# Optimization experiments

Measured on AMD Instinct MI355X. Metric: run time of the kernel, lower is better.

Reference implementation:

```python
import jax, jax.numpy as jnp
import numpy as np

VOCAB = 50257
EMBED_DIM = 768


def setup_inputs() -> dict:
    key = jax.random.key(0)
    k1, k2 = jax.random.split(key)
    x = jax.random.randint(k1, (8, 2048), 0, VOCAB, dtype=jnp.int64 if jax.config.jax_enable_x64 else jnp.int32)
    weight = jax.random.normal(k2, (EMBED_DIM, VOCAB), dtype=jnp.float32)
    return {"x": x, "weight": weight}


def reference(x, weight):
    # Original: one_hot(x, vocab) @ weight.T  ==  gather rows of weight.T
    # weight: [embed_dim, vocab]; output: [batch, seq, embed_dim]
    return jnp.take(weight.T, x, axis=0)
```

## Files before the change

### kernel.cpp

```cpp
#include <hip/hip_runtime.h>


#define VOCAB 50257
#define EMBED 768
#define WINB 32
#define NWIN 1571
#define NWIN_P 2048
#define RG 4
#define ROWS 192
#define LSTRIDE 33
#define CHUNK 256

__global__ __launch_bounds__(1024) void hist_scan_kernel(const int* __restrict__ x,
                                                         int n,
                                                         int* __restrict__ off,
                                                         int* __restrict__ cur) {
  __shared__ int h[NWIN_P];
  __shared__ int b[NWIN_P];
  const int t = threadIdx.x;
  h[t] = 0; h[t + 1024] = 0;
  __syncthreads();
  for (int i = t; i < n; i += 1024) atomicAdd(&h[x[i] >> 5], 1);
  __syncthreads();
  int* src = h; int* dst = b;
  for (int d = 1; d < NWIN_P; d <<= 1) {
    for (int i = t; i < NWIN_P; i += 1024)
      dst[i] = (i >= d) ? src[i] + src[i - d] : src[i];
    __syncthreads();
    int* tmp = src; src = dst; dst = tmp;
  }
  for (int i = t; i < NWIN_P; i += 1024) {
    int e = (i > 0) ? src[i - 1] : 0;
    off[i] = e;
    cur[i] = e;
  }
}

__global__ __launch_bounds__(256) void scatter_kernel(const int* __restrict__ x,
                                                      int* __restrict__ cur,
                                                      int* __restrict__ sorted,
                                                      int n) {
  int i = blockIdx.x * blockDim.x + threadIdx.x;
  if (i < n) {
    int v = x[i];
    int p = atomicAdd(&cur[v >> 5], 1);
    sorted[p] = (i << 5) | (v & 31);
  }
}

__device__ __forceinline__ int xcd_swizzle(int bid, int nwg) {
  const int NX = 8;
  int q = nwg / NX, r = nwg % NX;
  int xcd = bid % NX, idx = bid / NX;
  int base = (xcd < r) ? xcd * (q + 1) : r * (q + 1) + (xcd - r) * q;
  return base + idx;
}

__global__ __launch_bounds__(256) void gather_kernel(const float* __restrict__ w,
                                                     const int* __restrict__ off,
                                                     const int* __restrict__ sorted,
                                                     float* __restrict__ out) {
  __shared__ float lds[ROWS * LSTRIDE];
  __shared__ int toks[CHUNK];
  const int logical = xcd_swizzle(blockIdx.x, NWIN * RG);
  const int wid = logical % NWIN;
  const int rg  = logical / NWIN;
  const int row0 = rg * ROWS;
  const int col0 = wid * WINB;
  const int tid = threadIdx.x;

  int beg = off[wid], end = off[wid + 1];

  if (wid != NWIN - 1) {
    #pragma unroll
    for (int j = tid; j < ROWS * 8; j += 256) {
      int r = j >> 3, c4 = (j & 7) << 2;
      float4 v = *(const float4*)&w[(size_t)(row0 + r) * VOCAB + col0 + c4];
      float* d = &lds[r * LSTRIDE + c4];
      d[0] = v.x; d[1] = v.y; d[2] = v.z; d[3] = v.w;
    }
  } else {
    for (int j = tid; j < ROWS * 8; j += 256) {
      int r = j >> 3, c4 = (j & 7) << 2;
      float* d = &lds[r * LSTRIDE + c4];
      for (int u = 0; u < 4; ++u) {
        int c = col0 + c4 + u;
        d[u] = (c < VOCAB) ? w[(size_t)(row0 + r) * VOCAB + c] : 0.f;
      }
    }
  }

  int m = end - beg; if (m > CHUNK) m = CHUNK;
  if (tid < m) toks[tid] = sorted[beg + tid];
  __syncthreads();

  const int wave = tid >> 6, lane = tid & 63;
  while (true) {
    for (int i = wave; i < m; i += 4) {
      int pk = toks[i];
      int t = pk >> 5, c = pk & 31;
      float* o = &out[(size_t)t * EMBED + row0];
      #pragma unroll
      for (int k = 0; k < 3; ++k)
        o[k * 64 + lane] = lds[(k * 64 + lane) * LSTRIDE + c];
    }
    beg += m;
    if (beg >= end) break;
    __syncthreads();
    m = end - beg; if (m > CHUNK) m = CHUNK;
    if (tid < m) toks[tid] = sorted[beg + tid];
    __syncthreads();
  }
}

extern "C" void kernel_launch(void* const* d_in, const int* in_sizes, int n_in,
                              void* d_out, int out_size, void* d_ws, size_t ws_size,
                              hipStream_t stream) {
  const int*   x = (const int*)d_in[0];
  const float* w = (const float*)d_in[1];
  float* out = (float*)d_out;
  const int n = in_sizes[0];

  int* off    = (int*)d_ws;
  int* cur    = off + NWIN_P + 1;
  int* sorted = cur + NWIN_P;

  hist_scan_kernel<<<1, 1024, 0, stream>>>(x, n, off, cur);
  scatter_kernel<<<(n + 255) / 256, 256, 0, stream>>>(x, cur, sorted, n);
  gather_kernel<<<NWIN * RG, 256, 0, stream>>>(w, off, sorted, out);
}
```

Measured before the change: 52.51 us.

## Load weight tiles with direct global-to-LDS loads and XOR-swizzled layout

The gather kernel now stages weight tiles into LDS with global_load_lds 16-byte direct loads instead of register round-trips. The padded stride is replaced by an XOR swizzle to avoid bank conflicts, and the tile shrinks to 128 rows across 6 row groups. The histogram moves from one single-block kernel to a grid-wide atomic kernel plus a separate scan kernel and a memset. This adds two launches and relies on the direct-to-LDS lane/address mapping being correct.

Result: slower. 56.27 us (+7.2%).

```diff
diff --git a/kernel.cpp b/kernel.cpp
--- a/kernel.cpp
+++ b/kernel.cpp
@@ -6,23 +6,25 @@
 #define WINB 32
 #define NWIN 1571
 #define NWIN_P 2048
-#define RG 4
-#define ROWS 192
-#define LSTRIDE 33
+#define RG 6
+#define ROWS 128
 #define CHUNK 256
 
-__global__ __launch_bounds__(1024) void hist_scan_kernel(const int* __restrict__ x,
-                                                         int n,
-                                                         int* __restrict__ off,
-                                                         int* __restrict__ cur) {
-  __shared__ int h[NWIN_P];
-  __shared__ int b[NWIN_P];
-  const int t = threadIdx.x;
-  h[t] = 0; h[t + 1024] = 0;
+__global__ __launch_bounds__(256) void hist_kernel(const int* __restrict__ x,
+                                                   int* __restrict__ cnt, int n) {
+  int i = blockIdx.x * blockDim.x + threadIdx.x;
+  if (i < n) atomicAdd(&cnt[x[i] >> 5], 1);
+}
+
+__global__ __launch_bounds__(1024) void scan_kernel(const int* __restrict__ cnt,
+                                                    int* __restrict__ off,
+                                                    int* __restrict__ cur) {
+  __shared__ int a[NWIN_P], b[NWIN_P];
+  int t = threadIdx.x;
+  a[t] = cnt[t];
+  a[t + 1024] = cnt[t + 1024];
   __syncthreads();
-  for (int i = t; i < n; i += 1024) atomicAdd(&h[x[i] >> 5], 1);
-  __syncthreads();
-  int* src = h; int* dst = b;
+  int* src = a; int* dst = b;
   for (int d = 1; d < NWIN_P; d <<= 1) {
     for (int i = t; i < NWIN_P; i += 1024)
       dst[i] = (i >= d) ? src[i] + src[i - d] : src[i];
@@ -60,7 +62,7 @@
                                                      const int* __restrict__ off,
                                                      const int* __restrict__ sorted,
                                                      float* __restrict__ out) {
-  __shared__ float lds[ROWS * LSTRIDE];
+  __shared__ float lds[ROWS * WINB];
   __shared__ int toks[CHUNK];
   const int logical = xcd_swizzle(blockIdx.x, NWIN * RG);
   const int wid = logical % NWIN;
@@ -68,25 +70,28 @@
   const int row0 = rg * ROWS;
   const int col0 = wid * WINB;
   const int tid = threadIdx.x;
+  const int wave = tid >> 6, lane = tid & 63;
 
   int beg = off[wid], end = off[wid + 1];
 
   if (wid != NWIN - 1) {
     #pragma unroll
-    for (int j = tid; j < ROWS * 8; j += 256) {
-      int r = j >> 3, c4 = (j & 7) << 2;
-      float4 v = *(const float4*)&w[(size_t)(row0 + r) * VOCAB + col0 + c4];
-      float* d = &lds[r * LSTRIDE + c4];
-      d[0] = v.x; d[1] = v.y; d[2] = v.z; d[3] = v.w;
+    for (int k = 0; k < ROWS * 8 / 256; ++k) {
+      int p = k * 256 + tid;
+      int r = p >> 3;
+      int c4 = (p & 7) ^ ((r >> 2) & 7);
+      const float* src = &w[(size_t)(row0 + r) * VOCAB + col0 + (c4 << 2)];
+      float* dst = &lds[(k * 1024 + wave * 256)];
+      __builtin_amdgcn_global_load_lds(
+          (const __attribute__((address_space(1))) void*)src,
+          (__attribute__((address_space(3))) void*)dst, 16, 0, 0);
     }
   } else {
-    for (int j = tid; j < ROWS * 8; j += 256) {
-      int r = j >> 3, c4 = (j & 7) << 2;
-      float* d = &lds[r * LSTRIDE + c4];
-      for (int u = 0; u < 4; ++u) {
-        int c = col0 + c4 + u;
-        d[u] = (c < VOCAB) ? w[(size_t)(row0 + r) * VOCAB + c] : 0.f;
-      }
+    for (int j = tid; j < ROWS * WINB; j += 256) {
+      int r = j >> 5, cc = j & 31;
+      int c = col0 + cc;
+      float v = (c < VOCAB) ? w[(size_t)(row0 + r) * VOCAB + c] : 0.f;
+      lds[r * WINB + ((((cc >> 2) ^ ((r >> 2) & 7)) << 2) | (cc & 3))] = v;
     }
   }
 
@@ -94,15 +99,16 @@
   if (tid < m) toks[tid] = sorted[beg + tid];
   __syncthreads();
 
-  const int wave = tid >> 6, lane = tid & 63;
+  const int xorv = (lane >> 2) & 7;
   while (true) {
     for (int i = wave; i < m; i += 4) {
       int pk = toks[i];
-      int t = pk >> 5, c = pk & 31;
+      int t = pk >> 5, cc = pk & 31;
+      int slot = (((cc >> 2) ^ xorv) << 2) | (cc & 3);
       float* o = &out[(size_t)t * EMBED + row0];
       #pragma unroll
-      for (int k = 0; k < 3; ++k)
-        o[k * 64 + lane] = lds[(k * 64 + lane) * LSTRIDE + c];
+      for (int k = 0; k < ROWS / 64; ++k)
+        o[k * 64 + lane] = lds[(k * 64 + lane) * WINB + slot];
     }
     beg += m;
     if (beg >= end) break;
@@ -121,11 +127,14 @@
   float* out = (float*)d_out;
   const int n = in_sizes[0];
 
-  int* off    = (int*)d_ws;
-  int* cur    = off + NWIN_P + 1;
+  int* cnt    = (int*)d_ws;
+  int* off    = cnt + NWIN_P;
+  int* cur    = off + NWIN_P;
   int* sorted = cur + NWIN_P;
 
-  hist_scan_kernel<<<1, 1024, 0, stream>>>(x, n, off, cur);
+  hipMemsetAsync(cnt, 0, NWIN_P * sizeof(int), stream);
+  hist_kernel<<<(n + 255) / 256, 256, 0, stream>>>(x, cnt, n);
+  scan_kernel<<<1, 1024, 0, stream>>>(cnt, off, cur);
   scatter_kernel<<<(n + 255) / 256, 256, 0, stream>>>(x, cur, sorted, n);
   gather_kernel<<<NWIN * RG, 256, 0, stream>>>(w, off, sorted, out);
 }
```

## Fuse histogram/scatter into gather by having each block scan all tokens

Applied to the files above, without the earlier changes.

Drops the separate histogram-scan and scatter kernels. Each gather block now reads the whole token array (16K ints) and uses LDS atomics to collect the tokens that fall in its 32-column window, with a chunked fallback when a window holds more than 256 tokens. This removes two kernel launches, including a serial single-block scan, at the cost of every one of roughly 6.3K blocks re-reading the 64KB index array, mostly from cache.

Result: slower. 63.92 us (+21.7%).

```diff
diff --git a/kernel.cpp b/kernel.cpp
--- a/kernel.cpp
+++ b/kernel.cpp
@@ -5,48 +5,10 @@
 #define EMBED 768
 #define WINB 32
 #define NWIN 1571
-#define NWIN_P 2048
 #define RG 4
 #define ROWS 192
 #define LSTRIDE 33
-#define CHUNK 256
-
-__global__ __launch_bounds__(1024) void hist_scan_kernel(const int* __restrict__ x,
-                                                         int n,
-                                                         int* __restrict__ off,
-                                                         int* __restrict__ cur) {
-  __shared__ int h[NWIN_P];
-  __shared__ int b[NWIN_P];
-  const int t = threadIdx.x;
-  h[t] = 0; h[t + 1024] = 0;
-  __syncthreads();
-  for (int i = t; i < n; i += 1024) atomicAdd(&h[x[i] >> 5], 1);
-  __syncthreads();
-  int* src = h; int* dst = b;
-  for (int d = 1; d < NWIN_P; d <<= 1) {
-    for (int i = t; i < NWIN_P; i += 1024)
-      dst[i] = (i >= d) ? src[i] + src[i - d] : src[i];
-    __syncthreads();
-    int* tmp = src; src = dst; dst = tmp;
-  }
-  for (int i = t; i < NWIN_P; i += 1024) {
-    int e = (i > 0) ? src[i - 1] : 0;
-    off[i] = e;
-    cur[i] = e;
-  }
-}
-
-__global__ __launch_bounds__(256) void scatter_kernel(const int* __restrict__ x,
-                                                      int* __restrict__ cur,
-                                                      int* __restrict__ sorted,
-                                                      int n) {
-  int i = blockIdx.x * blockDim.x + threadIdx.x;
-  if (i < n) {
-    int v = x[i];
-    int p = atomicAdd(&cur[v >> 5], 1);
-    sorted[p] = (i << 5) | (v & 31);
-  }
-}
+#define CAP 256
 
 __device__ __forceinline__ int xcd_swizzle(int bid, int nwg) {
   const int NX = 8;
@@ -56,20 +18,23 @@
   return base + idx;
 }
 
-__global__ __launch_bounds__(256) void gather_kernel(const float* __restrict__ w,
-                                                     const int* __restrict__ off,
-                                                     const int* __restrict__ sorted,
-                                                     float* __restrict__ out) {
+__global__ __launch_bounds__(256) void embed_kernel(const int* __restrict__ x,
+                                                    const float* __restrict__ w,
+                                                    float* __restrict__ out,
+                                                    int n) {
   __shared__ float lds[ROWS * LSTRIDE];
-  __shared__ int toks[CHUNK];
+  __shared__ int toks[CAP];
+  __shared__ int cnt;
   const int logical = xcd_swizzle(blockIdx.x, NWIN * RG);
   const int wid = logical % NWIN;
   const int rg  = logical / NWIN;
   const int row0 = rg * ROWS;
   const int col0 = wid * WINB;
   const int tid = threadIdx.x;
+  const int wave = tid >> 6, lane = tid & 63;
 
-  int beg = off[wid], end = off[wid + 1];
+  if (tid == 0) cnt = 0;
+  __syncthreads();
 
   if (wid != NWIN - 1) {
     #pragma unroll
@@ -90,12 +55,24 @@
     }
   }
 
-  int m = end - beg; if (m > CHUNK) m = CHUNK;
-  if (tid < m) toks[tid] = sorted[beg + tid];
+  const int4* x4 = (const int4*)x;
+  const int n4 = n >> 2;
+  for (int j = tid; j < n4; j += 256) {
+    int4 v = x4[j];
+    int bt = j << 2;
+    if ((v.x >> 5) == wid) { int p = atomicAdd(&cnt, 1); if (p < CAP) toks[p] = ((bt    ) << 5) | (v.x & 31); }
+    if ((v.y >> 5) == wid) { int p = atomicAdd(&cnt, 1); if (p < CAP) toks[p] = ((bt + 1) << 5) | (v.y & 31); }
+    if ((v.z >> 5) == wid) { int p = atomicAdd(&cnt, 1); if (p < CAP) toks[p] = ((bt + 2) << 5) | (v.z & 31); }
+    if ((v.w >> 5) == wid) { int p = atomicAdd(&cnt, 1); if (p < CAP) toks[p] = ((bt + 3) << 5) | (v.w & 31); }
+  }
+  for (int j = (n4 << 2) + tid; j < n; j += 256) {
+    int v = x[j];
+    if ((v >> 5) == wid) { int p = atomicAdd(&cnt, 1); if (p < CAP) toks[p] = (j << 5) | (v & 31); }
+  }
   __syncthreads();
 
-  const int wave = tid >> 6, lane = tid & 63;
-  while (true) {
+  const int m = cnt;
+  if (m <= CAP) {
     for (int i = wave; i < m; i += 4) {
       int pk = toks[i];
       int t = pk >> 5, c = pk & 31;
@@ -104,12 +81,28 @@
       for (int k = 0; k < 3; ++k)
         o[k * 64 + lane] = lds[(k * 64 + lane) * LSTRIDE + c];
     }
-    beg += m;
-    if (beg >= end) break;
+  } else {
     __syncthreads();
-    m = end - beg; if (m > CHUNK) m = CHUNK;
-    if (tid < m) toks[tid] = sorted[beg + tid];
-    __syncthreads();
+    for (int c0 = 0; c0 < n; c0 += CAP) {
+      if (tid == 0) cnt = 0;
+      __syncthreads();
+      int c1 = (c0 + CAP < n) ? c0 + CAP : n;
+      for (int j = c0 + tid; j < c1; j += 256) {
+        int v = x[j];
+        if ((v >> 5) == wid) { int p = atomicAdd(&cnt, 1); toks[p] = (j << 5) | (v & 31); }
+      }
+      __syncthreads();
+      int mm = cnt;
+      for (int i = wave; i < mm; i += 4) {
+        int pk = toks[i];
+        int t = pk >> 5, c = pk & 31;
+        float* o = &out[(size_t)t * EMBED + row0];
+        #pragma unroll
+        for (int k = 0; k < 3; ++k)
+          o[k * 64 + lane] = lds[(k * 64 + lane) * LSTRIDE + c];
+      }
+      __syncthreads();
+    }
   }
 }
 
@@ -121,11 +114,5 @@
   float* out = (float*)d_out;
   const int n = in_sizes[0];
 
-  int* off    = (int*)d_ws;
-  int* cur    = off + NWIN_P + 1;
-  int* sorted = cur + NWIN_P;
-
-  hist_scan_kernel<<<1, 1024, 0, stream>>>(x, n, off, cur);
-  scatter_kernel<<<(n + 255) / 256, 256, 0, stream>>>(x, cur, sorted, n);
-  gather_kernel<<<NWIN * RG, 256, 0, stream>>>(w, off, sorted, out);
+  embed_kernel<<<NWIN * RG, 256, 0, stream>>>(x, w, out, n);
 }
```
